# Kernel tuning notes

Hardware: AMD Instinct MI355X
Metric: run time of the kernel (lower is better)

The kernel has to match this reference:

```python
import jax, jax.numpy as jnp
import numpy as np

NUM_PTS = 5      # num_points_per_it
MAX_IT = 25      # RANSAC iterations
TOL = 0.1        # inlier tolerance
G_PRIOR = 0.5    # bottom fraction of image assumed ground
VAX = 1          # vertical axis index


def get_AB(pts):
    """pts (..., 3) -> A (..., 3) = [non-vertical coords, 1], Bm (..., 1) = vertical coord."""
    Bm = pts[..., VAX:VAX + 1]
    cols = [pts[..., i:i + 1] for i in range(3) if i != VAX]
    A = jnp.concatenate(cols + [jnp.ones_like(Bm)], axis=-1)
    return A, Bm


def setup_inputs() -> dict:
    key = jax.random.key(0)
    k1, k2 = jax.random.split(key)
    B, H, W = 4, 384, 1280
    points = jax.random.normal(k1, (B, 3, H, W), dtype=jnp.float32)
    N = int(G_PRIOR * H) * W  # 245760 ground-candidate points per image
    T = NUM_PTS * MAX_IT      # 125 sampled indices per image
    rand_ind = jax.random.randint(k2, (B, T), 0, N, dtype=jnp.int32)
    return {"points": points, "rand_ind": rand_ind}


def reference(points, rand_ind):
    B, _, H, W = points.shape
    gH = int(G_PRIOR * H)
    N = gH * W
    # ground candidates: bottom half of image -> (B, N, 3)
    gp = points[:, :, H - gH:, :].reshape(B, 3, N).transpose(0, 2, 1)
    # gather RANSAC samples -> (B*MAX_IT, NUM_PTS, 3), b-major order (matches torch stack+reshape)
    sampled = jnp.take_along_axis(gp, rand_ind[..., None], axis=1).reshape(B * MAX_IT, NUM_PTS, 3)
    # least-squares plane fit per hypothesis: w = inv(A^T A + 1e-6) A^T b  (scalar 1e-6 added to ALL entries, faithful to torch)
    A, Bm = get_AB(sampled)
    At = jnp.swapaxes(A, 1, 2)
    ws = jnp.linalg.inv(At @ A + 1e-6) @ At @ Bm  # (B*MAX_IT, 3, 1)
    # NOTE: original code pairs ws (b-major) with points.repeat(max_it,1,1) (it-major);
    # we replicate that pairing exactly for faithfulness.
    ps = jnp.tile(gp, (MAX_IT, 1, 1))  # (MAX_IT*B, N, 3)
    Ap, Bp = get_AB(ps)
    abs_dist = jnp.abs(Ap @ ws - Bp).reshape(B, MAX_IT, N)
    # inlier voting + best hypothesis per image
    fit = (abs_dist < TOL).astype(jnp.float32).mean(axis=2)  # (B, MAX_IT)
    best = jnp.argmax(fit, axis=1)
    best_w = ws.reshape(B, MAX_IT, 3, 1)[jnp.arange(B), best]  # (B, 3, 1)
    # distance of every pixel to selected plane
    ap = points.reshape(B, 3, H * W).transpose(0, 2, 1)
    Aa, Ba = get_AB(ap)
    dist = (Aa @ best_w - Ba).transpose(0, 2, 1).reshape(B, 1, H, W)
    # forward returns detached tensors
    return jax.lax.stop_gradient(dist), jax.lax.stop_gradient(best_w)
```

## Files before the change

kernel.cpp:

```cpp
#include <hip/hip_runtime.h>
#include <hip/hip_bf16.h>


constexpr int BN      = 4;
constexpr int H       = 384;
constexpr int W       = 1280;
constexpr int HW      = H * W;
constexpr int GH      = 192;
constexpr int NPTS    = GH * W;
constexpr int MAX_IT  = 25;
constexpr int NUM_PTS = 5;
constexpr int TOTAL_P = BN * MAX_IT;

constexpr int NGRP         = 5;
constexpr int GSZ          = 5;
constexpr int CHUNKS       = 60;
constexpr int PSTRIDE      = 64;
constexpr int F4_PER_CHUNK = NPTS / 4 / CHUNKS;
constexpr int ITERS        = F4_PER_CHUNK / 256;
constexpr int BLOCKS_PER_B = (HW / 4) / 256;

__global__ __launch_bounds__(256) void k_count(
        const float* __restrict__ pts, const int* __restrict__ rind,
        float* __restrict__ wsf, int* __restrict__ partial) {
    __shared__ double swt[GSZ][3];
    __shared__ int    spid[GSZ];
    __shared__ int    sacc[GSZ];
    int grp   = blockIdx.x % NGRP;
    int pb    = (blockIdx.x / NGRP) % BN;
    int chunk = blockIdx.x / (NGRP * BN);
    int tid   = threadIdx.x;
    if (tid < GSZ) {
        sacc[tid] = 0;
        int target = grp * GSZ + tid;
        int s = 0, pi = 0;
        for (int b = 0; b < BN; ++b) {
            int r = ((pb - b) % BN + BN) % BN;
            for (int it = r; it < MAX_IT; it += BN) {
                if (s == target) pi = b * MAX_IT + it;
                ++s;
            }
        }
        spid[tid] = pi;
        int fb = pi / MAX_IT, fit_it = pi % MAX_IT;
        const float* base = pts + (size_t)fb * 3 * HW + (size_t)(H - GH) * W;
        const int* ri = rind + fb * (MAX_IT * NUM_PTS) + fit_it * NUM_PTS;
        double Sxx = 0, Sxz = 0, Sx = 0, Szz = 0, Sz = 0, Sxy = 0, Szy = 0, Sy = 0;
#pragma unroll
        for (int p = 0; p < NUM_PTS; ++p) {
            int n = ri[p];
            double x = (double)base[n];
            double y = (double)base[HW + n];
            double z = (double)base[2 * HW + n];
            Sxx += x * x; Sxz += x * z; Sx += x;
            Szz += z * z; Sz += z;
            Sxy += x * y; Szy += z * y; Sy += y;
        }
        const double e = 1e-6;
        double m00 = Sxx + e, m01 = Sxz + e, m02 = Sx + e;
        double m10 = Sxz + e, m11 = Szz + e, m12 = Sz + e;
        double m20 = Sx + e,  m21 = Sz + e,  m22 = (double)NUM_PTS + e;
        double v0 = Sxy, v1 = Szy, v2 = Sy;
        double det = m00 * (m11 * m22 - m12 * m21)
                   - m01 * (m10 * m22 - m12 * m20)
                   + m02 * (m10 * m21 - m11 * m20);
        double inv = 1.0 / det;
        double d0 = v0  * (m11 * m22 - m12 * m21)
                  - m01 * (v1  * m22 - m12 * v2 )
                  + m02 * (v1  * m21 - m11 * v2 );
        double d1 = m00 * (v1  * m22 - m12 * v2 )
                  - v0  * (m10 * m22 - m12 * m20)
                  + m02 * (m10 * v2  - v1  * m20);
        double d2 = m00 * (m11 * v2  - v1  * m21)
                  - m01 * (m10 * v2  - v1  * m20)
                  + v0  * (m10 * m21 - m11 * m20);
        double w0 = d0 * inv, w1 = d1 * inv, w2 = d2 * inv;
        swt[tid][0] = w0; swt[tid][1] = w1; swt[tid][2] = w2;
        if (chunk == 0) {
            wsf[pi * 3 + 0] = (float)w0;
            wsf[pi * 3 + 1] = (float)w1;
            wsf[pi * 3 + 2] = (float)w2;
        }
    }
    __syncthreads();
    double wa0 = swt[0][0], wa1 = swt[0][1], wa2 = swt[0][2];
    double wb0 = swt[1][0], wb1 = swt[1][1], wb2 = swt[1][2];
    double wc0 = swt[2][0], wc1 = swt[2][1], wc2 = swt[2][2];
    double wd0 = swt[3][0], wd1 = swt[3][1], wd2 = swt[3][2];
    double we0 = swt[4][0], we1 = swt[4][1], we2 = swt[4][2];

    const float* base = pts + (size_t)pb * 3 * HW + (size_t)(H - GH) * W;
    const float4* px = (const float4*)base;
    const float4* py = (const float4*)(base + HW);
    const float4* pz = (const float4*)(base + 2 * HW);

    int a0 = 0, a1 = 0, a2 = 0, a3 = 0, a4 = 0;
#pragma unroll
    for (int it = 0; it < ITERS; ++it) {
        int f = chunk * F4_PER_CHUNK + it * 256 + tid;
        float4 x4 = px[f], y4 = py[f], z4 = pz[f];
#pragma unroll
        for (int e = 0; e < 4; ++e) {
            double x = (double)((const float*)&x4)[e];
            double y = (double)((const float*)&y4)[e];
            double z = (double)((const float*)&z4)[e];
            double nb = -y;
            a0 += (fabs(fma(x, wa0, fma(z, wa1, wa2 + nb))) < 0.1) ? 1 : 0;
            a1 += (fabs(fma(x, wb0, fma(z, wb1, wb2 + nb))) < 0.1) ? 1 : 0;
            a2 += (fabs(fma(x, wc0, fma(z, wc1, wc2 + nb))) < 0.1) ? 1 : 0;
            a3 += (fabs(fma(x, wd0, fma(z, wd1, wd2 + nb))) < 0.1) ? 1 : 0;
            a4 += (fabs(fma(x, we0, fma(z, we1, we2 + nb))) < 0.1) ? 1 : 0;
        }
    }
    int vals[GSZ] = {a0, a1, a2, a3, a4};
#pragma unroll
    for (int j = 0; j < GSZ; ++j) {
        int v = vals[j];
        for (int off = 32; off > 0; off >>= 1) v += __shfl_down(v, off, 64);
        if ((tid & 63) == 0) atomicAdd(&sacc[j], v);
    }
    __syncthreads();
    if (tid < GSZ) partial[spid[tid] * PSTRIDE + chunk] = sacc[tid];
}

__global__ __launch_bounds__(256) void k_dist(
        const float* __restrict__ pts, const float* __restrict__ wsf,
        const int* __restrict__ partial, float* __restrict__ out) {
    __shared__ int   scnt[MAX_IT];
    __shared__ float sw[3];
    int b   = blockIdx.x / BLOCKS_PER_B;
    int blk = blockIdx.x % BLOCKS_PER_B;
    int tid = threadIdx.x;
    if (tid < MAX_IT) {
        const int* p = partial + (b * MAX_IT + tid) * PSTRIDE;
        int s = 0;
#pragma unroll
        for (int c = 0; c < CHUNKS; ++c) s += p[c];
        scnt[tid] = s;
    }
    __syncthreads();
    if (tid == 0) {
        int best = 0, bc = scnt[0];
        for (int it = 1; it < MAX_IT; ++it) {
            int c = scnt[it];
            if (c > bc) { bc = c; best = it; }
        }
        int pi = b * MAX_IT + best;
        sw[0] = wsf[pi * 3 + 0];
        sw[1] = wsf[pi * 3 + 1];
        sw[2] = wsf[pi * 3 + 2];
        if (blk == 0) {
            out[(size_t)BN * HW + b * 3 + 0] = sw[0];
            out[(size_t)BN * HW + b * 3 + 1] = sw[1];
            out[(size_t)BN * HW + b * 3 + 2] = sw[2];
        }
    }
    __syncthreads();
    float w0 = sw[0], w1 = sw[1], w2 = sw[2];
    const float4* px = (const float4*)(pts + (size_t)b * 3 * HW);
    const float4* py = px + HW / 4;
    const float4* pz = py + HW / 4;
    int i = blk * 256 + tid;
    float4 x = px[i], y = py[i], z = pz[i];
    float4 r;
    r.x = w0 * x.x + w1 * z.x + w2 - y.x;
    r.y = w0 * x.y + w1 * z.y + w2 - y.y;
    r.z = w0 * x.z + w1 * z.z + w2 - y.z;
    r.w = w0 * x.w + w1 * z.w + w2 - y.w;
    ((float4*)(out + (size_t)b * HW))[i] = r;
}

extern "C" void kernel_launch(void* const* d_in, const int* in_sizes, int n_in,
                              void* d_out, int out_size, void* d_ws, size_t ws_size,
                              hipStream_t stream) {
    const float* pts  = (const float*)d_in[0];
    const int*   rind = (const int*)d_in[1];
    float* out = (float*)d_out;

    float* wsf     = (float*)d_ws;
    int*   partial = (int*)(wsf + TOTAL_P * 3 + 4);

    k_count<<<NGRP * BN * CHUNKS, 256, 0, stream>>>(pts, rind, wsf, partial);
    k_dist <<<BN * BLOCKS_PER_B, 256, 0, stream>>>(pts, wsf, partial, out);
}
```

Measured before the change: 86.58 us.

## Test all 25 planes per block in fp32 and read each point chunk once

The inlier-count kernel now gives each block all 25 hypotheses for its image and a smaller chunk of points (120 chunks of 512 float4), instead of 5 plane groups that each re-read the points. The distance test runs in fp32 instead of fp64, which is meant to avoid slow double-precision arithmetic and cut redundant global reads. The cost is 25 counters and 75 weights held in registers per thread, which may lower occupancy. fp32 rounding could flip inlier decisions near the 0.1 tolerance and change which plane wins. The partial-sum reduction now reads with int4 loads.

```diff
diff --git a/kernel.cpp b/kernel.cpp
--- a/kernel.cpp
+++ b/kernel.cpp
@@ -1,5 +1,4 @@
 #include <hip/hip_runtime.h>
-#include <hip/hip_bf16.h>
 
 
 constexpr int BN      = 4;
@@ -12,32 +11,29 @@
 constexpr int NUM_PTS = 5;
 constexpr int TOTAL_P = BN * MAX_IT;
 
-constexpr int NGRP         = 5;
-constexpr int GSZ          = 5;
-constexpr int CHUNKS       = 60;
-constexpr int PSTRIDE      = 64;
-constexpr int F4_PER_CHUNK = NPTS / 4 / CHUNKS;
-constexpr int ITERS        = F4_PER_CHUNK / 256;
+constexpr int PLANES_PB    = 25;
+constexpr int CH_F4        = 512;
+constexpr int CHUNKS       = (NPTS / 4) / CH_F4;
+constexpr int ITERS        = CH_F4 / 256;
+constexpr int PSTRIDE      = 128;
 constexpr int BLOCKS_PER_B = (HW / 4) / 256;
 
 __global__ __launch_bounds__(256) void k_count(
         const float* __restrict__ pts, const int* __restrict__ rind,
         float* __restrict__ wsf, int* __restrict__ partial) {
-    __shared__ double swt[GSZ][3];
-    __shared__ int    spid[GSZ];
-    __shared__ int    sacc[GSZ];
-    int grp   = blockIdx.x % NGRP;
-    int pb    = (blockIdx.x / NGRP) % BN;
-    int chunk = blockIdx.x / (NGRP * BN);
+    __shared__ float sw[PLANES_PB][3];
+    __shared__ int   spid[PLANES_PB];
+    __shared__ int   sacc[PLANES_PB];
+    int pb    = blockIdx.x & 3;
+    int chunk = blockIdx.x >> 2;
     int tid   = threadIdx.x;
-    if (tid < GSZ) {
+    if (tid < PLANES_PB) {
         sacc[tid] = 0;
-        int target = grp * GSZ + tid;
         int s = 0, pi = 0;
         for (int b = 0; b < BN; ++b) {
             int r = ((pb - b) % BN + BN) % BN;
             for (int it = r; it < MAX_IT; it += BN) {
-                if (s == target) pi = b * MAX_IT + it;
+                if (s == tid) pi = b * MAX_IT + it;
                 ++s;
             }
         }
@@ -75,7 +71,7 @@
                   - m01 * (m10 * v2  - v1  * m20)
                   + v0  * (m10 * m21 - m11 * m20);
         double w0 = d0 * inv, w1 = d1 * inv, w2 = d2 * inv;
-        swt[tid][0] = w0; swt[tid][1] = w1; swt[tid][2] = w2;
+        sw[tid][0] = (float)w0; sw[tid][1] = (float)w1; sw[tid][2] = (float)w2;
         if (chunk == 0) {
             wsf[pi * 3 + 0] = (float)w0;
             wsf[pi * 3 + 1] = (float)w1;
@@ -83,44 +79,45 @@
         }
     }
     __syncthreads();
-    double wa0 = swt[0][0], wa1 = swt[0][1], wa2 = swt[0][2];
-    double wb0 = swt[1][0], wb1 = swt[1][1], wb2 = swt[1][2];
-    double wc0 = swt[2][0], wc1 = swt[2][1], wc2 = swt[2][2];
-    double wd0 = swt[3][0], wd1 = swt[3][1], wd2 = swt[3][2];
-    double we0 = swt[4][0], we1 = swt[4][1], we2 = swt[4][2];
+    float w0[PLANES_PB], w1[PLANES_PB], w2[PLANES_PB];
+#pragma unroll
+    for (int p = 0; p < PLANES_PB; ++p) {
+        w0[p] = sw[p][0]; w1[p] = sw[p][1]; w2[p] = sw[p][2];
+    }
 
     const float* base = pts + (size_t)pb * 3 * HW + (size_t)(H - GH) * W;
     const float4* px = (const float4*)base;
     const float4* py = (const float4*)(base + HW);
     const float4* pz = (const float4*)(base + 2 * HW);
 
-    int a0 = 0, a1 = 0, a2 = 0, a3 = 0, a4 = 0;
+    int cnt[PLANES_PB];
+#pragma unroll
+    for (int p = 0; p < PLANES_PB; ++p) cnt[p] = 0;
+
 #pragma unroll
     for (int it = 0; it < ITERS; ++it) {
-        int f = chunk * F4_PER_CHUNK + it * 256 + tid;
+        int f = chunk * CH_F4 + it * 256 + tid;
         float4 x4 = px[f], y4 = py[f], z4 = pz[f];
 #pragma unroll
         for (int e = 0; e < 4; ++e) {
-            double x = (double)((const float*)&x4)[e];
-            double y = (double)((const float*)&y4)[e];
-            double z = (double)((const float*)&z4)[e];
-            double nb = -y;
-            a0 += (fabs(fma(x, wa0, fma(z, wa1, wa2 + nb))) < 0.1) ? 1 : 0;
-            a1 += (fabs(fma(x, wb0, fma(z, wb1, wb2 + nb))) < 0.1) ? 1 : 0;
-            a2 += (fabs(fma(x, wc0, fma(z, wc1, wc2 + nb))) < 0.1) ? 1 : 0;
-            a3 += (fabs(fma(x, wd0, fma(z, wd1, wd2 + nb))) < 0.1) ? 1 : 0;
-            a4 += (fabs(fma(x, we0, fma(z, we1, we2 + nb))) < 0.1) ? 1 : 0;
+            float x = ((const float*)&x4)[e];
+            float y = ((const float*)&y4)[e];
+            float z = ((const float*)&z4)[e];
+#pragma unroll
+            for (int p = 0; p < PLANES_PB; ++p) {
+                float d = fmaf(x, w0[p], fmaf(z, w1[p], w2[p] - y));
+                cnt[p] += (fabsf(d) < 0.1f) ? 1 : 0;
+            }
         }
     }
-    int vals[GSZ] = {a0, a1, a2, a3, a4};
 #pragma unroll
-    for (int j = 0; j < GSZ; ++j) {
-        int v = vals[j];
+    for (int p = 0; p < PLANES_PB; ++p) {
+        int v = cnt[p];
         for (int off = 32; off > 0; off >>= 1) v += __shfl_down(v, off, 64);
-        if ((tid & 63) == 0) atomicAdd(&sacc[j], v);
+        if ((tid & 63) == 0) atomicAdd(&sacc[p], v);
     }
     __syncthreads();
-    if (tid < GSZ) partial[spid[tid] * PSTRIDE + chunk] = sacc[tid];
+    if (tid < PLANES_PB) partial[spid[tid] * PSTRIDE + chunk] = sacc[tid];
 }
 
 __global__ __launch_bounds__(256) void k_dist(
@@ -132,10 +129,13 @@
     int blk = blockIdx.x % BLOCKS_PER_B;
     int tid = threadIdx.x;
     if (tid < MAX_IT) {
-        const int* p = partial + (b * MAX_IT + tid) * PSTRIDE;
+        const int4* p = (const int4*)(partial + (b * MAX_IT + tid) * PSTRIDE);
         int s = 0;
 #pragma unroll
-        for (int c = 0; c < CHUNKS; ++c) s += p[c];
+        for (int c = 0; c < CHUNKS / 4; ++c) {
+            int4 v = p[c];
+            s += v.x + v.y + v.z + v.w;
+        }
         scnt[tid] = s;
     }
     __syncthreads();
@@ -180,6 +180,6 @@
     float* wsf     = (float*)d_ws;
     int*   partial = (int*)(wsf + TOTAL_P * 3 + 4);
 
-    k_count<<<NGRP * BN * CHUNKS, 256, 0, stream>>>(pts, rind, wsf, partial);
+    k_count<<<BN * CHUNKS, 256, 0, stream>>>(pts, rind, wsf, partial);
     k_dist <<<BN * BLOCKS_PER_B, 256, 0, stream>>>(pts, wsf, partial, out);
 }
```

Measured after the change: 85.63 us. No clear change (-1.1%).
